# Performance work log

Hardware: AMD Instinct MI355X
Metric: run time of the kernel (lower is better)

## Reference

```python
import jax, jax.numpy as jnp
import numpy as np

BN_EPS = 1e-5
N_IN, N_OUT, K, CIN, COUT = 2_000_000, 250_000, 8, 32, 64


def setup_inputs() -> dict:
    key = jax.random.key(0)
    k1, k2, k3 = jax.random.split(key, 3)
    x = jax.random.normal(k1, (N_IN, CIN), dtype=jnp.float32)
    neigh = jax.random.randint(k2, (N_OUT, K), 0, N_IN, dtype=jnp.int64)
    weight = jax.random.normal(k3, (K, CIN, COUT), dtype=jnp.float32) * 0.05
    gamma = jnp.ones((COUT,), dtype=jnp.float32)
    beta = jnp.zeros((COUT,), dtype=jnp.float32)
    return {"x": x, "neigh": neigh, "weight": weight, "gamma": gamma, "beta": beta}


def reference(x, neigh, weight, gamma, beta):
    # Octree conv (nempty=True, stride 2): gather K child-octant features, GEMM.
    gathered = x[neigh]                      # [N_out, K, Cin]
    out = jnp.einsum('nkc,kcd->nd', gathered, weight)  # [N_out, Cout]
    # BatchNorm1d (training mode: batch statistics over octants)
    mean = jnp.mean(out, axis=0)
    var = jnp.var(out, axis=0)
    y = (out - mean) * jax.lax.rsqrt(var + BN_EPS) * gamma + beta
    return y
```

## Files before the change

### kernel.cpp

```cpp
#include <hip/hip_runtime.h>
#include <hip/hip_bf16.h>

#define N_OUT_ROWS 250000
#define TILES 15625
#define NBLK 512
#define WPB 4
#define NWAVES (NBLK * WPB)
#define BN_EPS 1e-5f

typedef __attribute__((ext_vector_type(8))) short bf16x8;
typedef __attribute__((ext_vector_type(8))) unsigned short u16x8;
typedef __attribute__((ext_vector_type(4))) float f32x4;

static __device__ __forceinline__ unsigned short f2bf(float f) {
  union { float f; unsigned u; } v; v.f = f;
  unsigned r = v.u + 0x7FFFu + ((v.u >> 16) & 1u);
  return (unsigned short)(r >> 16);
}

#define GLOAD_LDS16(gsrc, ldst)                                                \
  __builtin_amdgcn_global_load_lds(                                            \
      (const __attribute__((address_space(1))) unsigned int*)(gsrc),           \
      (__attribute__((address_space(3))) unsigned int*)(ldst), 16, 0, 0)

__global__ void k_prep(const float* __restrict__ w,
                       unsigned short* __restrict__ bfrag,
                       float* __restrict__ stats) {
  const int i = blockIdx.x * 256 + threadIdx.x;
  if (i < 128) stats[i] = 0.f;
  const int f = i >> 6, l = i & 63;
  const int kt = f >> 2, ct = f & 3, rr = l & 15, gg = l >> 4;
  u16x8 o;
  #pragma unroll
  for (int j = 0; j < 8; ++j)
    o[j] = f2bf(w[(kt * 32 + gg * 8 + j) * 64 + ct * 16 + rr]);
  *reinterpret_cast<u16x8*>(bfrag + i * 8) = o;
}

__global__ __launch_bounds__(256, 2)
void k_gemm(const float* __restrict__ x, const int* __restrict__ neigh,
            const unsigned short* __restrict__ bfrag, float* __restrict__ out,
            float* __restrict__ stats) {
  __shared__ __align__(16) unsigned char Abuf_all[WPB][16384];
  __shared__ float wpart[WPB][128];

  const int tid = threadIdx.x;
  const int lane = tid & 63;
  const int widx = tid >> 6;
  unsigned char* Abuf = Abuf_all[widx];

  bf16x8 bf[8][4];
  #pragma unroll
  for (int kt = 0; kt < 8; ++kt)
    #pragma unroll
    for (int ct = 0; ct < 4; ++ct)
      bf[kt][ct] = *reinterpret_cast<const bf16x8*>(
          bfrag + ((kt * 4 + ct) * 64 + lane) * 8);

  const int gw = blockIdx.x * WPB + widx;
  const int q = TILES / NWAVES;
  const int rem = TILES % NWAVES;
  const int start = (gw < rem) ? gw * (q + 1) : rem * (q + 1) + (gw - rem) * q;
  const int cnt = q + (gw < rem ? 1 : 0);

  const int r = lane & 15;
  const int g4 = lane >> 4;
  const int seg = lane & 7;
  const int ktl = lane >> 3;
  const int swz = (r & 7) << 4;
  const int rdbase = (r << 10) + (g4 << 5);

  float sacc[4] = {0.f, 0.f, 0.f, 0.f};
  float qacc[4] = {0.f, 0.f, 0.f, 0.f};

  for (int k = 0; k < cnt; ++k) {
    const int t = start + k;
    const int n0 = t << 4;

    int idxv[16];
    #pragma unroll
    for (int m = 0; m < 16; ++m)
      idxv[m] = neigh[(n0 + m) * 8 + ktl];

    asm volatile("s_waitcnt lgkmcnt(0)" ::: "memory");
    __builtin_amdgcn_sched_barrier(0);

    #pragma unroll
    for (int j = 0; j < 16; ++j) {
      const float* src = x + (size_t)idxv[j] * 32 + ((seg ^ (j & 7)) * 4);
      GLOAD_LDS16(src, Abuf + j * 1024);
    }

    asm volatile("s_waitcnt vmcnt(0)" ::: "memory");
    __builtin_amdgcn_sched_barrier(0);

    f32x4 acc[4];
    #pragma unroll
    for (int ct = 0; ct < 4; ++ct) acc[ct] = (f32x4){0.f, 0.f, 0.f, 0.f};

    #pragma unroll
    for (int kt = 0; kt < 8; ++kt) {
      const int o0 = rdbase + (kt << 7);
      const f32x4 a0 = *reinterpret_cast<const f32x4*>(Abuf + (o0 ^ swz));
      const f32x4 a1 = *reinterpret_cast<const f32x4*>(Abuf + ((o0 + 16) ^ swz));
      union { bf16x8 v; __hip_bfloat162 h[4]; } af;
      af.h[0] = __float22bfloat162_rn(make_float2(a0[0], a0[1]));
      af.h[1] = __float22bfloat162_rn(make_float2(a0[2], a0[3]));
      af.h[2] = __float22bfloat162_rn(make_float2(a1[0], a1[1]));
      af.h[3] = __float22bfloat162_rn(make_float2(a1[2], a1[3]));
      #pragma unroll
      for (int ct = 0; ct < 4; ++ct)
        acc[ct] = __builtin_amdgcn_mfma_f32_16x16x32_bf16(af.v, bf[kt][ct],
                                                          acc[ct], 0, 0, 0);
    }

    const int rbase = n0 + g4 * 4;
    #pragma unroll
    for (int ct = 0; ct < 4; ++ct) {
      #pragma unroll
      for (int j = 0; j < 4; ++j)
        out[(rbase + j) * 64 + ct * 16 + r] = acc[ct][j];
      sacc[ct] += acc[ct][0] + acc[ct][1] + acc[ct][2] + acc[ct][3];
      qacc[ct] += acc[ct][0] * acc[ct][0] + acc[ct][1] * acc[ct][1] +
                  acc[ct][2] * acc[ct][2] + acc[ct][3] * acc[ct][3];
    }
  }

  #pragma unroll
  for (int ct = 0; ct < 4; ++ct) {
    sacc[ct] += __shfl_xor(sacc[ct], 16);
    qacc[ct] += __shfl_xor(qacc[ct], 16);
    sacc[ct] += __shfl_xor(sacc[ct], 32);
    qacc[ct] += __shfl_xor(qacc[ct], 32);
  }
  if (lane < 16) {
    #pragma unroll
    for (int ct = 0; ct < 4; ++ct) {
      wpart[widx][ct * 16 + lane] = sacc[ct];
      wpart[widx][64 + ct * 16 + lane] = qacc[ct];
    }
  }
  __syncthreads();
  if (tid < 128) {
    atomicAdd(&stats[tid], wpart[0][tid] + wpart[1][tid] +
                           wpart[2][tid] + wpart[3][tid]);
  }
}

__global__ __launch_bounds__(256)
void k_bn(float* __restrict__ out, const float* __restrict__ stats,
          const float* __restrict__ gamma, const float* __restrict__ beta) {
  __shared__ float sc[64], bs[64];
  if (threadIdx.x < 64) {
    const int d = threadIdx.x;
    const float inv = 1.0f / (float)N_OUT_ROWS;
    const float mean = stats[d] * inv;
    const float var = stats[64 + d] * inv - mean * mean;
    const float rstd = rsqrtf(var + BN_EPS);
    const float scale = rstd * gamma[d];
    sc[d] = scale;
    bs[d] = beta[d] - mean * scale;
  }
  __syncthreads();

  const int total4 = N_OUT_ROWS * 64 / 4;
  float4* o4 = reinterpret_cast<float4*>(out);
  for (int i = blockIdx.x * blockDim.x + threadIdx.x; i < total4;
       i += gridDim.x * blockDim.x) {
    const int d0 = (i & 15) << 2;
    float4 v = o4[i];
    v.x = v.x * sc[d0]     + bs[d0];
    v.y = v.y * sc[d0 + 1] + bs[d0 + 1];
    v.z = v.z * sc[d0 + 2] + bs[d0 + 2];
    v.w = v.w * sc[d0 + 3] + bs[d0 + 3];
    o4[i] = v;
  }
}

extern "C" void kernel_launch(void* const* d_in, const int* in_sizes, int n_in,
                              void* d_out, int out_size, void* d_ws, size_t ws_size,
                              hipStream_t stream) {
  const float* x     = (const float*)d_in[0];
  const int*   neigh = (const int*)d_in[1];
  const float* w     = (const float*)d_in[2];
  const float* gamma = (const float*)d_in[3];
  const float* beta  = (const float*)d_in[4];
  float* out = (float*)d_out;

  float* stats = (float*)d_ws;
  unsigned short* bfrag = (unsigned short*)((char*)d_ws + 1024);

  k_prep<<<8, 256, 0, stream>>>(w, bfrag, stats);
  k_gemm<<<NBLK, 256, 0, stream>>>(x, neigh, bfrag, out, stats);
  k_bn<<<2048, 256, 0, stream>>>(out, stats, gamma, beta);
}
```

Before: 85.52 us.

## Double-buffer gather into LDS with prefetched neighbor indices per wave

Turns the per-wave gather into a software pipeline. Tile k+1's feature rows are loaded straight from global memory into a second LDS buffer while tile k is computed, and neighbor indices are read two tiles ahead and handed out with shuffles. Partial waitcnt values keep the wave from stalling on the whole gather. To fit the doubled LDS it halves the grid and drops to one block per CU, and it replaces the block-level stats reduction with per-wave atomics. The cost is lower occupancy and more atomic traffic.

```diff
diff --git a/kernel.cpp b/kernel.cpp
--- a/kernel.cpp
+++ b/kernel.cpp
@@ -3,10 +3,12 @@
 
 #define N_OUT_ROWS 250000
 #define TILES 15625
-#define NBLK 512
+#define NBLK 256
 #define WPB 4
 #define NWAVES (NBLK * WPB)
 #define BN_EPS 1e-5f
+
+#define SB() __builtin_amdgcn_sched_barrier(0)
 
 typedef __attribute__((ext_vector_type(8))) short bf16x8;
 typedef __attribute__((ext_vector_type(8))) unsigned short u16x8;
@@ -37,17 +39,16 @@
   *reinterpret_cast<u16x8*>(bfrag + i * 8) = o;
 }
 
-__global__ __launch_bounds__(256, 2)
+__global__ __launch_bounds__(256, 1)
 void k_gemm(const float* __restrict__ x, const int* __restrict__ neigh,
             const unsigned short* __restrict__ bfrag, float* __restrict__ out,
             float* __restrict__ stats) {
-  __shared__ __align__(16) unsigned char Abuf_all[WPB][16384];
-  __shared__ float wpart[WPB][128];
+  __shared__ __align__(16) unsigned char Abuf_all[WPB][2][16384];
 
   const int tid = threadIdx.x;
   const int lane = tid & 63;
   const int widx = tid >> 6;
-  unsigned char* Abuf = Abuf_all[widx];
+  unsigned char* Abuf = &Abuf_all[widx][0][0];
 
   bf16x8 bf[8][4];
   #pragma unroll
@@ -70,30 +71,52 @@
   const int swz = (r & 7) << 4;
   const int rdbase = (r << 10) + (g4 << 5);
 
+  auto LDIDX = [&](int t, int& a, int& b) {
+    const int tt = (t < TILES) ? t : (TILES - 1);
+    const int* p = neigh + tt * 128;
+    a = p[lane];
+    b = p[64 + lane];
+  };
+  auto ISSUE = [&](int bsel, int a, int b) {
+    unsigned char* B = Abuf + (bsel << 14);
+    #pragma unroll
+    for (int j = 0; j < 16; ++j) {
+      const int id = __shfl((j < 8) ? a : b, ((j & 7) << 3) + ktl, 64);
+      const float* src = x + (size_t)id * 32 + ((seg ^ (j & 7)) << 2);
+      GLOAD_LDS16(src, B + j * 1024);
+    }
+  };
+
   float sacc[4] = {0.f, 0.f, 0.f, 0.f};
   float qacc[4] = {0.f, 0.f, 0.f, 0.f};
 
+  int cA, cB, pA, pB, nA, nB;
+  LDIDX(start, cA, cB);
+  LDIDX(start + 1, pA, pB);
+  SB();
+  ISSUE(0, cA, cB);
+  SB();
+  LDIDX(start + 2, nA, nB);
+  SB();
+
   for (int k = 0; k < cnt; ++k) {
-    const int t = start + k;
-    const int n0 = t << 4;
-
-    int idxv[16];
-    #pragma unroll
-    for (int m = 0; m < 16; ++m)
-      idxv[m] = neigh[(n0 + m) * 8 + ktl];
-
-    asm volatile("s_waitcnt lgkmcnt(0)" ::: "memory");
-    __builtin_amdgcn_sched_barrier(0);
-
-    #pragma unroll
-    for (int j = 0; j < 16; ++j) {
-      const float* src = x + (size_t)idxv[j] * 32 + ((seg ^ (j & 7)) * 4);
-      GLOAD_LDS16(src, Abuf + j * 1024);
-    }
-
-    asm volatile("s_waitcnt vmcnt(0)" ::: "memory");
-    __builtin_amdgcn_sched_barrier(0);
-
+    if (k + 1 < cnt) {
+      asm volatile("s_waitcnt lgkmcnt(0)" ::: "memory");
+      SB();
+      ISSUE((k + 1) & 1, pA, pB);
+      SB();
+      int zA, zB;
+      LDIDX(start + k + 3, zA, zB);
+      SB();
+      pA = nA; pB = nB; nA = zA; nB = zB;
+    }
+
+    if (k == cnt - 1)      asm volatile("s_waitcnt vmcnt(0)" ::: "memory");
+    else if (k == 0)       asm volatile("s_waitcnt vmcnt(18)" ::: "memory");
+    else                   asm volatile("s_waitcnt vmcnt(34)" ::: "memory");
+    SB();
+
+    const unsigned char* B = Abuf + ((k & 1) << 14);
     f32x4 acc[4];
     #pragma unroll
     for (int ct = 0; ct < 4; ++ct) acc[ct] = (f32x4){0.f, 0.f, 0.f, 0.f};
@@ -101,8 +124,8 @@
     #pragma unroll
     for (int kt = 0; kt < 8; ++kt) {
       const int o0 = rdbase + (kt << 7);
-      const f32x4 a0 = *reinterpret_cast<const f32x4*>(Abuf + (o0 ^ swz));
-      const f32x4 a1 = *reinterpret_cast<const f32x4*>(Abuf + ((o0 + 16) ^ swz));
+      const f32x4 a0 = *reinterpret_cast<const f32x4*>(B + (o0 ^ swz));
+      const f32x4 a1 = *reinterpret_cast<const f32x4*>(B + ((o0 + 16) ^ swz));
       union { bf16x8 v; __hip_bfloat162 h[4]; } af;
       af.h[0] = __float22bfloat162_rn(make_float2(a0[0], a0[1]));
       af.h[1] = __float22bfloat162_rn(make_float2(a0[2], a0[3]));
@@ -114,7 +137,7 @@
                                                           acc[ct], 0, 0, 0);
     }
 
-    const int rbase = n0 + g4 * 4;
+    const int rbase = ((start + k) << 4) + g4 * 4;
     #pragma unroll
     for (int ct = 0; ct < 4; ++ct) {
       #pragma unroll
@@ -136,14 +159,9 @@
   if (lane < 16) {
     #pragma unroll
     for (int ct = 0; ct < 4; ++ct) {
-      wpart[widx][ct * 16 + lane] = sacc[ct];
-      wpart[widx][64 + ct * 16 + lane] = qacc[ct];
-    }
-  }
-  __syncthreads();
-  if (tid < 128) {
-    atomicAdd(&stats[tid], wpart[0][tid] + wpart[1][tid] +
-                           wpart[2][tid] + wpart[3][tid]);
+      atomicAdd(&stats[ct * 16 + lane], sacc[ct]);
+      atomicAdd(&stats[64 + ct * 16 + lane], qacc[ct]);
+    }
   }
 }
 
```

Measured after the change: 97.82 us. 1.14x slower.

## Store GEMM intermediate as bf16 in workspace and coalesce neighbor index loads

Applied to the files above, without the earlier changes.

The GEMM kernel can now write its pre-normalization output as bf16 into workspace instead of fp32 into the output buffer. The BN kernel then reads bf16 and writes fp32, which roughly halves the intermediate write and read traffic. Neighbor indices are loaded with two coalesced loads per wave and spread with shuffles instead of 16 strided loads, and the per-block LDS reduction of stats is replaced by direct per-wave atomics. The bf16 rounding of the intermediate adds precision error, and the bf16 path runs only if the workspace is large enough.

```diff
diff --git a/kernel.cpp b/kernel.cpp
--- a/kernel.cpp
+++ b/kernel.cpp
@@ -8,6 +8,8 @@
 #define NWAVES (NBLK * WPB)
 #define BN_EPS 1e-5f
 
+#define SB() __builtin_amdgcn_sched_barrier(0)
+
 typedef __attribute__((ext_vector_type(8))) short bf16x8;
 typedef __attribute__((ext_vector_type(8))) unsigned short u16x8;
 typedef __attribute__((ext_vector_type(4))) float f32x4;
@@ -16,6 +18,10 @@
   union { float f; unsigned u; } v; v.f = f;
   unsigned r = v.u + 0x7FFFu + ((v.u >> 16) & 1u);
   return (unsigned short)(r >> 16);
+}
+static __device__ __forceinline__ float bf2f(unsigned short s) {
+  union { unsigned u; float f; } v; v.u = ((unsigned)s) << 16;
+  return v.f;
 }
 
 #define GLOAD_LDS16(gsrc, ldst)                                                \
@@ -37,12 +43,13 @@
   *reinterpret_cast<u16x8*>(bfrag + i * 8) = o;
 }
 
+template <bool BF16OUT>
 __global__ __launch_bounds__(256, 2)
 void k_gemm(const float* __restrict__ x, const int* __restrict__ neigh,
-            const unsigned short* __restrict__ bfrag, float* __restrict__ out,
+            const unsigned short* __restrict__ bfrag,
+            float* __restrict__ outf, unsigned short* __restrict__ outb,
             float* __restrict__ stats) {
   __shared__ __align__(16) unsigned char Abuf_all[WPB][16384];
-  __shared__ float wpart[WPB][128];
 
   const int tid = threadIdx.x;
   const int lane = tid & 63;
@@ -77,22 +84,22 @@
     const int t = start + k;
     const int n0 = t << 4;
 
-    int idxv[16];
-    #pragma unroll
-    for (int m = 0; m < 16; ++m)
-      idxv[m] = neigh[(n0 + m) * 8 + ktl];
+    const int* p = neigh + t * 128;
+    const int ia = p[lane];
+    const int ib = p[64 + lane];
 
     asm volatile("s_waitcnt lgkmcnt(0)" ::: "memory");
-    __builtin_amdgcn_sched_barrier(0);
+    SB();
 
     #pragma unroll
     for (int j = 0; j < 16; ++j) {
-      const float* src = x + (size_t)idxv[j] * 32 + ((seg ^ (j & 7)) * 4);
+      const int id = __shfl((j < 8) ? ia : ib, ((j & 7) << 3) + ktl, 64);
+      const float* src = x + (size_t)id * 32 + ((seg ^ (j & 7)) << 2);
       GLOAD_LDS16(src, Abuf + j * 1024);
     }
 
     asm volatile("s_waitcnt vmcnt(0)" ::: "memory");
-    __builtin_amdgcn_sched_barrier(0);
+    SB();
 
     f32x4 acc[4];
     #pragma unroll
@@ -118,8 +125,11 @@
     #pragma unroll
     for (int ct = 0; ct < 4; ++ct) {
       #pragma unroll
-      for (int j = 0; j < 4; ++j)
-        out[(rbase + j) * 64 + ct * 16 + r] = acc[ct][j];
+      for (int j = 0; j < 4; ++j) {
+        const int off = (rbase + j) * 64 + ct * 16 + r;
+        if (BF16OUT) outb[off] = f2bf(acc[ct][j]);
+        else         outf[off] = acc[ct][j];
+      }
       sacc[ct] += acc[ct][0] + acc[ct][1] + acc[ct][2] + acc[ct][3];
       qacc[ct] += acc[ct][0] * acc[ct][0] + acc[ct][1] * acc[ct][1] +
                   acc[ct][2] * acc[ct][2] + acc[ct][3] * acc[ct][3];
@@ -136,20 +146,17 @@
   if (lane < 16) {
     #pragma unroll
     for (int ct = 0; ct < 4; ++ct) {
-      wpart[widx][ct * 16 + lane] = sacc[ct];
-      wpart[widx][64 + ct * 16 + lane] = qacc[ct];
-    }
-  }
-  __syncthreads();
-  if (tid < 128) {
-    atomicAdd(&stats[tid], wpart[0][tid] + wpart[1][tid] +
-                           wpart[2][tid] + wpart[3][tid]);
-  }
-}
-
+      atomicAdd(&stats[ct * 16 + lane], sacc[ct]);
+      atomicAdd(&stats[64 + ct * 16 + lane], qacc[ct]);
+    }
+  }
+}
+
+template <bool BF16IN>
 __global__ __launch_bounds__(256)
-void k_bn(float* __restrict__ out, const float* __restrict__ stats,
-          const float* __restrict__ gamma, const float* __restrict__ beta) {
+void k_bn(float* __restrict__ out, const unsigned short* __restrict__ inb,
+          const float* __restrict__ stats, const float* __restrict__ gamma,
+          const float* __restrict__ beta) {
   __shared__ float sc[64], bs[64];
   if (threadIdx.x < 64) {
     const int d = threadIdx.x;
@@ -163,17 +170,37 @@
   }
   __syncthreads();
 
-  const int total4 = N_OUT_ROWS * 64 / 4;
-  float4* o4 = reinterpret_cast<float4*>(out);
-  for (int i = blockIdx.x * blockDim.x + threadIdx.x; i < total4;
-       i += gridDim.x * blockDim.x) {
-    const int d0 = (i & 15) << 2;
-    float4 v = o4[i];
-    v.x = v.x * sc[d0]     + bs[d0];
-    v.y = v.y * sc[d0 + 1] + bs[d0 + 1];
-    v.z = v.z * sc[d0 + 2] + bs[d0 + 2];
-    v.w = v.w * sc[d0 + 3] + bs[d0 + 3];
-    o4[i] = v;
+  if (BF16IN) {
+    const int total8 = N_OUT_ROWS * 64 / 8;
+    for (int i = blockIdx.x * blockDim.x + threadIdx.x; i < total8;
+         i += gridDim.x * blockDim.x) {
+      const int d0 = (i & 7) << 3;
+      const u16x8 v = *reinterpret_cast<const u16x8*>(inb + i * 8);
+      float4 o0, o1;
+      o0.x = bf2f(v[0]) * sc[d0 + 0] + bs[d0 + 0];
+      o0.y = bf2f(v[1]) * sc[d0 + 1] + bs[d0 + 1];
+      o0.z = bf2f(v[2]) * sc[d0 + 2] + bs[d0 + 2];
+      o0.w = bf2f(v[3]) * sc[d0 + 3] + bs[d0 + 3];
+      o1.x = bf2f(v[4]) * sc[d0 + 4] + bs[d0 + 4];
+      o1.y = bf2f(v[5]) * sc[d0 + 5] + bs[d0 + 5];
+      o1.z = bf2f(v[6]) * sc[d0 + 6] + bs[d0 + 6];
+      o1.w = bf2f(v[7]) * sc[d0 + 7] + bs[d0 + 7];
+      reinterpret_cast<float4*>(out)[i * 2] = o0;
+      reinterpret_cast<float4*>(out)[i * 2 + 1] = o1;
+    }
+  } else {
+    const int total4 = N_OUT_ROWS * 64 / 4;
+    float4* o4 = reinterpret_cast<float4*>(out);
+    for (int i = blockIdx.x * blockDim.x + threadIdx.x; i < total4;
+         i += gridDim.x * blockDim.x) {
+      const int d0 = (i & 15) << 2;
+      float4 v = o4[i];
+      v.x = v.x * sc[d0]     + bs[d0];
+      v.y = v.y * sc[d0 + 1] + bs[d0 + 1];
+      v.z = v.z * sc[d0 + 2] + bs[d0 + 2];
+      v.w = v.w * sc[d0 + 3] + bs[d0 + 3];
+      o4[i] = v;
+    }
   }
 }
 
@@ -189,8 +216,17 @@
 
   float* stats = (float*)d_ws;
   unsigned short* bfrag = (unsigned short*)((char*)d_ws + 1024);
+  unsigned short* obf = (unsigned short*)((char*)d_ws + 65536);
+
+  const bool bf16path =
+      ws_size >= (size_t)65536 + (size_t)N_OUT_ROWS * 64 * 2;
 
   k_prep<<<8, 256, 0, stream>>>(w, bfrag, stats);
-  k_gemm<<<NBLK, 256, 0, stream>>>(x, neigh, bfrag, out, stats);
-  k_bn<<<2048, 256, 0, stream>>>(out, stats, gamma, beta);
-}
+  if (bf16path) {
+    k_gemm<true><<<NBLK, 256, 0, stream>>>(x, neigh, bfrag, nullptr, obf, stats);
+    k_bn<true><<<2048, 256, 0, stream>>>(out, obf, stats, gamma, beta);
+  } else {
+    k_gemm<false><<<NBLK, 256, 0, stream>>>(x, neigh, bfrag, out, nullptr, stats);
+    k_bn<false><<<2048, 256, 0, stream>>>(out, nullptr, stats, gamma, beta);
+  }
+}
```

Measured after the change: 113.2 us. 32.4% more time.
